# Optimization experiments

Measured on AMD Instinct MI355X. Metric: run time of the kernel, lower is better.

## Reference

```python
import jax, jax.numpy as jnp
import numpy as np

HID = 2048; NH = 16; NKV = 2; HD = 128; G = NH // NKV
SEC = (16, 24, 24)  # sums to 64 = HD/2
EPS = 1e-6
B, S = 2, 1024


def _reorder(table):
    # table: [3, B, S, HD]; interleave sections picking axis i%3 per chunk
    chunks = []
    idx = 0
    for _ in range(2):
        for sec in SEC:
            chunks.append(table[..., idx:idx + sec])
            idx += sec
    return jnp.concatenate([c[i % len(SEC)] for i, c in enumerate(chunks)], axis=-1)  # [B,S,HD]


def rotate_half(x):
    x1, x2 = jnp.split(x, 2, axis=-1)
    return jnp.concatenate((-x2, x1), axis=-1)


def rms_norm(x, gamma):
    var = jnp.mean(jnp.square(x), axis=-1, keepdims=True)
    return gamma * (x * jax.lax.rsqrt(var + EPS))


def setup_inputs() -> dict:
    key = jax.random.key(0)
    ks = jax.random.split(key, 12)
    x = jax.random.normal(ks[0], (B, S, HID), dtype=jnp.float32)
    ang = jax.random.uniform(ks[1], (3, B, S, HD), dtype=jnp.float32) * 6.28318
    cos = jnp.cos(ang)
    sin = jnp.sin(ang)
    mask = jnp.ones((B, S), dtype=jnp.float32)
    sc = 0.02
    q_w = jax.random.normal(ks[2], (HID, NH * HD), dtype=jnp.float32) * sc
    q_b = jnp.zeros((NH * HD,), dtype=jnp.float32)
    k_w = jax.random.normal(ks[3], (HID, NKV * HD), dtype=jnp.float32) * sc
    k_b = jnp.zeros((NKV * HD,), dtype=jnp.float32)
    v_w = jax.random.normal(ks[4], (HID, NKV * HD), dtype=jnp.float32) * sc
    v_b = jnp.zeros((NKV * HD,), dtype=jnp.float32)
    q_gamma = jnp.ones((HD,), dtype=jnp.float32)
    k_gamma = jnp.ones((HD,), dtype=jnp.float32)
    o_w = jax.random.normal(ks[5], (NH * HD, HID), dtype=jnp.float32) * sc
    return {"x": x, "cos": cos, "sin": sin, "mask": mask,
            "q_w": q_w, "q_b": q_b, "k_w": k_w, "k_b": k_b,
            "v_w": v_w, "v_b": v_b, "q_gamma": q_gamma, "k_gamma": k_gamma,
            "o_w": o_w}


def reference(x, cos, sin, mask, q_w, q_b, k_w, k_b, v_w, v_b, q_gamma, k_gamma, o_w):
    b, s, _ = x.shape
    # QKV projections
    q = (x @ q_w + q_b).reshape(b, s, NH, HD)
    k = (x @ k_w + k_b).reshape(b, s, NKV, HD)
    v = (x @ v_w + v_b).reshape(b, s, NKV, HD)
    # per-head RMSNorm on q, k
    q = rms_norm(q, q_gamma)
    k = rms_norm(k, k_gamma)
    q = jnp.transpose(q, (0, 2, 1, 3))  # [B,NH,S,HD]
    k = jnp.transpose(k, (0, 2, 1, 3))  # [B,NKV,S,HD]
    v = jnp.transpose(v, (0, 2, 1, 3))
    # multimodal RoPE
    cos_f = _reorder(cos)[:, None, :, :]  # [B,1,S,HD]
    sin_f = _reorder(sin)[:, None, :, :]
    q = q * cos_f + rotate_half(q) * sin_f
    k = k * cos_f + rotate_half(k) * sin_f
    # key-mask zeroing and effective lengths
    eff = mask.sum(axis=-1).astype(jnp.int32)  # [B]
    bm = mask[:, None, :, None]
    k = k * bm
    v = v * bm
    hist = (jnp.arange(s)[None, :] < eff[:, None]).astype(jnp.float32)  # [B,S]
    # GQA attention scores in fp32
    qg = q.reshape(b, NKV, G, s, HD)
    scores = jnp.einsum('bngqd,bnkd->bngqk', qg, k,
                        precision=jax.lax.Precision.HIGHEST) * (HD ** -0.5)
    scores = scores.reshape(b, NH, s, s)
    scores = scores + (1.0 - hist)[:, None, None, :] * -1e9
    causal = jnp.tril(jnp.ones((s, s), dtype=jnp.float32))
    scores = scores + (1.0 - causal)[None, None, :, :] * -1e9
    aw = jax.nn.softmax(scores, axis=-1)
    # weighted values
    out = jnp.einsum('bngqk,bnkd->bngqd', aw.reshape(b, NKV, G, s, s), v,
                     precision=jax.lax.Precision.HIGHEST)
    out = out.reshape(b, NH, s, HD)
    out = jnp.transpose(out, (0, 2, 1, 3)).reshape(b, s, NH * HD)
    return out @ o_w
```

## Files before the change

### kernel.cpp

```cpp
#include <hip/hip_runtime.h>

typedef __attribute__((ext_vector_type(8))) short bf16x8;
typedef __attribute__((ext_vector_type(4))) float f32x4;

#define MFMA16(a, b, c) __builtin_amdgcn_mfma_f32_16x16x32_bf16(a, b, c, 0, 0, 0)

__device__ inline short f2bf(float f) {
  union { float f; unsigned u; } v;
  v.f = f;
  unsigned r = v.u + 0x7FFF + ((v.u >> 16) & 1);
  return (short)(r >> 16);
}
__device__ inline float bf2f(short s) {
  union { unsigned u; float f; } v;
  v.u = ((unsigned)(unsigned short)s) << 16;
  return v.f;
}
#define GLD_LDS16(g, l)                                                        \
  __builtin_amdgcn_global_load_lds(                                            \
      (const __attribute__((address_space(1))) unsigned int*)(g),              \
      (__attribute__((address_space(3))) unsigned int*)(l), 16, 0, 0)

__device__ __forceinline__ void raw_barrier() {
  __asm__ volatile("" ::: "memory");
  __builtin_amdgcn_s_barrier();
  __asm__ volatile("" ::: "memory");
}

__global__ __launch_bounds__(256) void prep_kernel(
    const float* __restrict__ x, const float* __restrict__ q_w,
    const float* __restrict__ k_w, const float* __restrict__ v_w,
    const float* __restrict__ o_w, short* __restrict__ xb,
    short* __restrict__ wqkv_t, short* __restrict__ wo_t) {
  __shared__ float t[64][65];
  int bid = blockIdx.x;
  if (bid < 4096) {
    int i = (bid * 256 + threadIdx.x) * 4;
    float4 f = *(const float4*)&x[i];
    short4 o;
    o.x = f2bf(f.x); o.y = f2bf(f.y); o.z = f2bf(f.z); o.w = f2bf(f.w);
    *(short4*)&xb[i] = o;
    return;
  }
  bid -= 4096;
  const float* src;
  short* dst;
  int C, bx, by;
  if (bid < 1024) {
    src = q_w; dst = wqkv_t; C = 2048;
    bx = (bid & 31) * 64; by = (bid >> 5) * 64;
  } else if (bid < 1152) {
    bid -= 1024;
    src = k_w; dst = wqkv_t + (size_t)2048 * 2048; C = 256;
    bx = (bid & 3) * 64; by = (bid >> 2) * 64;
  } else if (bid < 1280) {
    bid -= 1152;
    src = v_w; dst = wqkv_t + (size_t)2304 * 2048; C = 256;
    bx = (bid & 3) * 64; by = (bid >> 2) * 64;
  } else {
    bid -= 1280;
    src = o_w; dst = wo_t; C = 2048;
    bx = (bid & 31) * 64; by = (bid >> 5) * 64;
  }
  const int R = 2048;
  const int tx = threadIdx.x & 15;
  const int ty = threadIdx.x >> 4;
#pragma unroll
  for (int i = 0; i < 4; i++) {
    int row = ty + i * 16;
    float4 f = *(const float4*)&src[(size_t)(by + row) * C + bx + tx * 4];
    t[row][tx * 4 + 0] = f.x;
    t[row][tx * 4 + 1] = f.y;
    t[row][tx * 4 + 2] = f.z;
    t[row][tx * 4 + 3] = f.w;
  }
  __syncthreads();
#pragma unroll
  for (int i = 0; i < 4; i++) {
    int c = ty + i * 16;
    short4 o;
    o.x = f2bf(t[tx * 4 + 0][c]);
    o.y = f2bf(t[tx * 4 + 1][c]);
    o.z = f2bf(t[tx * 4 + 2][c]);
    o.w = f2bf(t[tx * 4 + 3][c]);
    *(short4*)&dst[(size_t)(bx + c) * R + by + tx * 4] = o;
  }
}

__global__ __launch_bounds__(256) void gemm_db_kernel(const short* __restrict__ A,
                                                      const short* __restrict__ B,
                                                      float* __restrict__ C, int N,
                                                      int gx, int gy) {
  __shared__ __align__(16) short As[4][64 * 32];
  __shared__ __align__(16) short Bs[4][128 * 32];
  const int bid = blockIdx.x;
  const int xcd = bid & 7, idx = bid >> 3;
  const int colsPerX = gx >> 1, rowsPerX = gy >> 2;
  const int xt = (xcd & 1) * colsPerX + idx % colsPerX;
  const int yt = (xcd >> 1) * rowsPerX + idx / colsPerX;
  const int tid = threadIdx.x;
  const int lane = tid & 63, wave = tid >> 6;
  const int quad = lane >> 4, l16 = lane & 15;
  const int m0 = yt * 64, n0 = xt * 128;
  const int wm = (wave >> 1) * 32, wn = (wave & 1) * 64;
  const int r0 = tid >> 2, c0 = (tid & 3) * 8;
  const int ca = c0 ^ ((r0 & 3) << 3);
  const size_t arow = (size_t)(m0 + r0) * 2048;
  const size_t brow0 = (size_t)(n0 + r0) * 2048, brow1 = (size_t)(n0 + r0 + 64) * 2048;
  f32x4 acc[2][4];
#pragma unroll
  for (int mi = 0; mi < 2; mi++)
#pragma unroll
    for (int ni = 0; ni < 4; ni++) acc[mi][ni] = (f32x4){0.f, 0.f, 0.f, 0.f};

#pragma unroll
  for (int st = 0; st < 4; st++) {
    const int kk = st * 32 + ca;
    GLD_LDS16(&A[arow + kk], &As[st][r0 * 32 + c0]);
    GLD_LDS16(&B[brow0 + kk], &Bs[st][r0 * 32 + c0]);
    GLD_LDS16(&B[brow1 + kk], &Bs[st][(r0 + 64) * 32 + c0]);
  }

  const int sx = (l16 & 3) << 3;
  for (int p = 0; p < 32; p++) {
    if (p < 31) {
      __asm__ volatile("s_waitcnt vmcnt(6)" ::: "memory");
    } else {
      __asm__ volatile("s_waitcnt vmcnt(0)" ::: "memory");
    }
    raw_barrier();
#pragma unroll
    for (int j = 0; j < 2; j++) {
      const int cur = (2 * p + j) & 3;
      bf16x8 af[2], bfr[4];
#pragma unroll
      for (int mi = 0; mi < 2; mi++)
        af[mi] = *(const bf16x8*)&As[cur][(wm + mi * 16 + l16) * 32 + ((quad * 8) ^ sx)];
#pragma unroll
      for (int ni = 0; ni < 4; ni++)
        bfr[ni] = *(const bf16x8*)&Bs[cur][(wn + ni * 16 + l16) * 32 + ((quad * 8) ^ sx)];
#pragma unroll
      for (int mi = 0; mi < 2; mi++)
#pragma unroll
        for (int ni = 0; ni < 4; ni++)
          acc[mi][ni] = MFMA16(af[mi], bfr[ni], acc[mi][ni]);
    }
    __asm__ volatile("s_waitcnt lgkmcnt(0)" ::: "memory");
    raw_barrier();
    if (p < 30) {
#pragma unroll
      for (int j = 0; j < 2; j++) {
        const int st = 2 * p + 4 + j;
        const int slot = st & 3;
        const int kk = st * 32 + ca;
        GLD_LDS16(&A[arow + kk], &As[slot][r0 * 32 + c0]);
        GLD_LDS16(&B[brow0 + kk], &Bs[slot][r0 * 32 + c0]);
        GLD_LDS16(&B[brow1 + kk], &Bs[slot][(r0 + 64) * 32 + c0]);
      }
    }
  }
#pragma unroll
  for (int mi = 0; mi < 2; mi++)
#pragma unroll
    for (int ni = 0; ni < 4; ni++)
#pragma unroll
      for (int r = 0; r < 4; r++)
        C[(size_t)(m0 + wm + mi * 16 + quad * 4 + r) * N + n0 + wn + ni * 16 + l16] =
            acc[mi][ni][r];
}

__global__ __launch_bounds__(256) void postv_kernel(
    const float* __restrict__ qkv, const float* __restrict__ qbias,
    const float* __restrict__ kbias, const float* __restrict__ vbias,
    const float* __restrict__ qg, const float* __restrict__ kg,
    const float* __restrict__ cosb, const float* __restrict__ sinb,
    const float* __restrict__ maskp, short* __restrict__ qo, short* __restrict__ ko,
    short* __restrict__ vtb) {
  __shared__ short t[32][33];
  const int bid = blockIdx.x;
  if (bid < 9216) {
    const int rid = bid * 4 + (threadIdx.x >> 6);
    const int lane = threadIdx.x & 63;
    const int slot = rid >> 11;
    const int bs = rid & 2047;
    const int b = bs >> 10, s = bs & 1023;
    const float* row = qkv + (size_t)bs * 2560;
    int off;
    const float* bias;
    const float* gamma;
    if (slot < 16) { off = slot * 128; bias = qbias + slot * 128; gamma = qg; }
    else { off = 2048 + (slot - 16) * 128; bias = kbias + (slot - 16) * 128; gamma = kg; }
    float v0 = row[off + lane] + bias[lane];
    float v1 = row[off + 64 + lane] + bias[64 + lane];
    float ss = v0 * v0 + v1 * v1;
#pragma unroll
    for (int o = 1; o < 64; o <<= 1) ss += __shfl_xor(ss, o);
    float r = rsqrtf(ss * (1.0f / 128.0f) + 1e-6f);
    v0 = gamma[lane] * v0 * r;
    v1 = gamma[64 + lane] * v1 * r;
    int sel = (lane < 16) ? 0 : (lane < 40) ? 1 : 2;
    size_t ci = ((size_t)(sel * 2 + b) * 1024 + s) * 128 + lane;
    float c0 = cosb[ci], s0 = sinb[ci], c1 = cosb[ci + 64], s1 = sinb[ci + 64];
    float o0 = v0 * c0 - v1 * s0;
    float o1 = v1 * c1 + v0 * s1;
    if (slot >= 16) { float mk = maskp[bs]; o0 *= mk; o1 *= mk; }
    size_t oidx;
    short* optr;
    if (slot < 16) { oidx = (((size_t)(b * 16 + slot) * 1024) + s) * 128; optr = qo; }
    else { oidx = (((size_t)(b * 2 + (slot - 16)) * 1024) + s) * 128; optr = ko; }
    optr[oidx + lane] = f2bf(o0);
    optr[oidx + 64 + lane] = f2bf(o1);
    return;
  }
  const int b2 = bid - 9216;
  const int d0 = (b2 & 3) * 32;
  const int s0 = ((b2 >> 2) & 31) * 32;
  const int bz = b2 >> 7;
  const int bq = bz >> 1, kv = bz & 1;
  const int tx = threadIdx.x & 31;
  const int ty = threadIdx.x >> 5;
#pragma unroll
  for (int i = 0; i < 4; i++) {
    int s = s0 + ty + i * 8;
    float val = qkv[((size_t)(bq * 1024 + s)) * 2560 + 2304 + kv * 128 + d0 + tx] +
                vbias[kv * 128 + d0 + tx];
    t[ty + i * 8][tx] = f2bf(val * maskp[bq * 1024 + s]);
  }
  __syncthreads();
#pragma unroll
  for (int i = 0; i < 4; i++)
    vtb[((size_t)bz * 128 + d0 + ty + i * 8) * 1024 + s0 + tx] = t[tx][ty + i * 8];
}

__global__ __launch_bounds__(256) void attn_kernel(const short* __restrict__ Q,
                                                   const short* __restrict__ K,
                                                   const short* __restrict__ Vt_g,
                                                   short* __restrict__ po,
                                                   float* __restrict__ pml) {
  int x = blockIdx.x;
  const int h = blockIdx.y;
  const int b = blockIdx.z;
  int g = 0, base = 0;
  while (x >= base + 4 * (g + 1)) { base += 4 * (g + 1); g++; }
  const int r0 = x - base;
  const int qt = 4 * g + r0 / (g + 1);
  const int kc = r0 % (g + 1);
  int nsteps = qt - 4 * kc + 1;
  if (nsteps > 4) nsteps = 4;

  const int kv = h >> 3;
  const int tid = threadIdx.x;
  const int wave = tid >> 6, lane = tid & 63;
  const int quad = lane >> 4, l16 = lane & 15;
  __shared__ __align__(16) short Ks[2][64 * 128];
  __shared__ __align__(16) short Vs[2][128 * 64];
  __shared__ __align__(16) short Ps[4][16 * 72];

  const size_t qoff = (((size_t)(b * 16 + h) * 1024) + qt * 64 + wave * 16 + l16) * 128;
  bf16x8 aq[4];
#pragma unroll
  for (int kk = 0; kk < 4; kk++) aq[kk] = *(const bf16x8*)&Q[qoff + kk * 32 + quad * 8];

  f32x4 o[8];
#pragma unroll
  for (int i = 0; i < 8; i++) o[i] = (f32x4){0.f, 0.f, 0.f, 0.f};
  float l[4] = {0.f, 0.f, 0.f, 0.f};
  const int qrow0 = qt * 64 + wave * 16 + quad * 4;
  const size_t koff = ((size_t)(b * 2 + kv) * 1024) * 128;
  const size_t voff = koff;
  const float scale = 0.08838834764831845f;

#define STAGE_KV(bf, ks0)                                                          \
  {                                                                                \
    _Pragma("unroll") for (int it = 0; it < 4; it++) {                             \
      const int c = it * 256 + tid;                                                \
      const int row = c >> 4, sl = c & 15;                                         \
      GLD_LDS16(&K[koff + (size_t)((ks0) + row) * 128 + ((sl ^ (row & 7)) * 8)],   \
                &Ks[bf][c * 8]);                                                   \
      const int d = c >> 3, sv = c & 7;                                            \
      GLD_LDS16(&Vt_g[voff + (size_t)d * 1024 + (ks0) + ((sv ^ (d & 7)) * 8)],     \
                &Vs[bf][c * 8]);                                                   \
    }                                                                              \
  }

  STAGE_KV(0, kc * 256);

  for (int st = 0; st < nsteps; st++) {
    __asm__ volatile("s_waitcnt vmcnt(0)" ::: "memory");
    raw_barrier();
    if (st + 1 < nsteps) { STAGE_KV((st + 1) & 1, kc * 256 + (st + 1) * 64); }
    const int cb = st & 1;
    const int ks0 = kc * 256 + st * 64;
    f32x4 sc[4];
#pragma unroll
    for (int nt = 0; nt < 4; nt++) sc[nt] = (f32x4){0.f, 0.f, 0.f, 0.f};
#pragma unroll
    for (int nt = 0; nt < 4; nt++) {
      const int rr = nt * 16 + l16;
#pragma unroll
      for (int kk = 0; kk < 4; kk++) {
        bf16x8 bk = *(const bf16x8*)&Ks[cb][rr * 128 + (((kk * 4 + quad) ^ (rr & 7)) * 8)];
        sc[nt] = MFMA16(aq[kk], bk, sc[nt]);
      }
    }
    short* P = &Ps[wave][0];
#pragma unroll
    for (int nt = 0; nt < 4; nt++) {
      const int kcol = ks0 + nt * 16 + l16;
#pragma unroll
      for (int r = 0; r < 4; r++) {
        float p = (kcol > qrow0 + r) ? 0.f : __expf(fmaf(sc[nt][r], scale, -12.0f));
        l[r] += p;
        P[(quad * 4 + r) * 72 + nt * 16 + l16] = f2bf(p);
      }
    }
    __asm__ volatile("s_waitcnt lgkmcnt(0)" ::: "memory");
    bf16x8 pa0 = *(const bf16x8*)&P[l16 * 72 + quad * 8];
    bf16x8 pa1 = *(const bf16x8*)&P[l16 * 72 + 32 + quad * 8];
#pragma unroll
    for (int nt = 0; nt < 8; nt++) {
      const int rr = nt * 16 + l16;
      bf16x8 bv0 = *(const bf16x8*)&Vs[cb][rr * 64 + ((quad ^ (rr & 7)) * 8)];
      bf16x8 bv1 = *(const bf16x8*)&Vs[cb][rr * 64 + (((4 + quad) ^ (rr & 7)) * 8)];
      o[nt] = MFMA16(pa0, bv0, o[nt]);
      o[nt] = MFMA16(pa1, bv1, o[nt]);
    }
  }
#undef STAGE_KV
#pragma unroll
  for (int off = 1; off < 16; off <<= 1)
#pragma unroll
    for (int r = 0; r < 4; r++) l[r] += __shfl_xor(l[r], off);
  const int p = (b * 16 + h) * 40 + blockIdx.x;
  const int lrow = wave * 16 + quad * 4;
#pragma unroll
  for (int nt = 0; nt < 8; nt++)
#pragma unroll
    for (int r = 0; r < 4; r++)
      po[(size_t)p * 8192 + (size_t)(lrow + r) * 128 + nt * 16 + l16] = f2bf(o[nt][r]);
  if (l16 == 0) {
#pragma unroll
    for (int r = 0; r < 4; r++) pml[(size_t)p * 64 + lrow + r] = l[r];
  }
}

__global__ __launch_bounds__(256) void attn_combine_kernel(const short* __restrict__ po,
                                                           const float* __restrict__ pml,
                                                           short* __restrict__ attn) {
  const int qt = blockIdx.x, h = blockIdx.y, b = blockIdx.z;
  const int g = qt >> 2, nc = g + 1;
  const int x0 = 2 * g * (g + 1) + (qt & 3) * nc;
  const int row = threadIdx.x >> 2;
  const int d0 = (threadIdx.x & 3) * 32;
  const int pbase = (b * 16 + h) * 40 + x0;
  float denom = 0.f;
#pragma unroll
  for (int kc = 0; kc < 4; kc++)
    if (kc < nc) denom += pml[(size_t)(pbase + kc) * 64 + row];
  float inv = 1.f / denom;
  float acc[32];
#pragma unroll
  for (int j = 0; j < 32; j++) acc[j] = 0.f;
#pragma unroll
  for (int kc = 0; kc < 4; kc++)
    if (kc < nc) {
      const short* src = po + (size_t)(pbase + kc) * 8192 + (size_t)row * 128 + d0;
#pragma unroll
      for (int j = 0; j < 4; j++) {
        int4 v = *(const int4*)&src[j * 8];
        const short* vs = (const short*)&v;
#pragma unroll
        for (int e = 0; e < 8; e++) acc[j * 8 + e] += bf2f(vs[e]);
      }
    }
  short ob[32];
#pragma unroll
  for (int j = 0; j < 32; j++) ob[j] = f2bf(acc[j] * inv);
  short* dst = attn + ((size_t)(b * 1024 + qt * 64 + row)) * 2048 + h * 128 + d0;
#pragma unroll
  for (int j = 0; j < 4; j++) *(int4*)&dst[j * 8] = *(const int4*)&ob[j * 8];
}

extern "C" void kernel_launch(void* const* d_in, const int* in_sizes, int n_in,
                              void* d_out, int out_size, void* d_ws, size_t ws_size,
                              hipStream_t stream) {
  const float* x = (const float*)d_in[0];
  const float* cosb = (const float*)d_in[1];
  const float* sinb = (const float*)d_in[2];
  const float* mask = (const float*)d_in[3];
  const float* q_w = (const float*)d_in[4];
  const float* q_b = (const float*)d_in[5];
  const float* k_w = (const float*)d_in[6];
  const float* k_b = (const float*)d_in[7];
  const float* v_w = (const float*)d_in[8];
  const float* v_b = (const float*)d_in[9];
  const float* qg = (const float*)d_in[10];
  const float* kg = (const float*)d_in[11];
  const float* o_w = (const float*)d_in[12];
  float* out = (float*)d_out;

  char* ws = (char*)d_ws;
  short* wo_t = (short*)(ws);
  short* wqkv_t = (short*)(ws + ((size_t)8 << 20));
  float* pml = (float*)(ws + ((size_t)8 << 20));
  short* attn = (short*)(ws + ((size_t)9 << 20));
  short* xb = (short*)(ws + ((size_t)18 << 20));
  short* qb = xb;
  float* qkv_raw = (float*)(ws + ((size_t)26 << 20));
  short* po = (short*)(ws + ((size_t)26 << 20));
  short* kb = (short*)(ws + ((size_t)46 << 20));
  short* vtb = (short*)(ws + ((size_t)47 << 20));

  prep_kernel<<<6400, 256, 0, stream>>>(x, q_w, k_w, v_w, o_w, xb, wqkv_t, wo_t);
  gemm_db_kernel<<<640, 256, 0, stream>>>(xb, wqkv_t, qkv_raw, 2560, 20, 32);
  postv_kernel<<<9728, 256, 0, stream>>>(qkv_raw, q_b, k_b, v_b, qg, kg, cosb, sinb, mask,
                                         qb, kb, vtb);
  attn_kernel<<<dim3(40, 16, 2), 256, 0, stream>>>(qb, kb, vtb, po, pml);
  attn_combine_kernel<<<dim3(16, 16, 2), 256, 0, stream>>>(po, pml, attn);
  gemm_db_kernel<<<512, 256, 0, stream>>>(attn, wo_t, out, 2048, 16, 32);
}
```

Before: 223.9 us.

## Split-K the QKV GEMM into two halves and change LDS swizzle pattern

```diff
diff --git a/kernel.cpp b/kernel.cpp
--- a/kernel.cpp
+++ b/kernel.cpp
@@ -89,11 +89,18 @@
 
 __global__ __launch_bounds__(256) void gemm_db_kernel(const short* __restrict__ A,
                                                       const short* __restrict__ B,
-                                                      float* __restrict__ C, int N,
-                                                      int gx, int gy) {
+                                                      float* __restrict__ C,
+                                                      float* __restrict__ C2, int N,
+                                                      int gx, int gy, int P) {
   __shared__ __align__(16) short As[4][64 * 32];
   __shared__ __align__(16) short Bs[4][128 * 32];
-  const int bid = blockIdx.x;
+  int bid = blockIdx.x;
+  const int gxy = gx * gy;
+  int half = 0;
+  if (bid >= gxy) { half = 1; bid -= gxy; }
+  float* __restrict__ Cw = half ? C2 : C;
+  const short* __restrict__ Ab = A + half * (P * 64);
+  const short* __restrict__ Bb = B + half * (P * 64);
   const int xcd = bid & 7, idx = bid >> 3;
   const int colsPerX = gx >> 1, rowsPerX = gy >> 2;
   const int xt = (xcd & 1) * colsPerX + idx % colsPerX;
@@ -104,7 +111,7 @@
   const int m0 = yt * 64, n0 = xt * 128;
   const int wm = (wave >> 1) * 32, wn = (wave & 1) * 64;
   const int r0 = tid >> 2, c0 = (tid & 3) * 8;
-  const int ca = c0 ^ ((r0 & 3) << 3);
+  const int ca = ((tid & 3) ^ ((r0 >> 1) & 3)) * 8;
   const size_t arow = (size_t)(m0 + r0) * 2048;
   const size_t brow0 = (size_t)(n0 + r0) * 2048, brow1 = (size_t)(n0 + r0 + 64) * 2048;
   f32x4 acc[2][4];
@@ -116,14 +123,14 @@
 #pragma unroll
   for (int st = 0; st < 4; st++) {
     const int kk = st * 32 + ca;
-    GLD_LDS16(&A[arow + kk], &As[st][r0 * 32 + c0]);
-    GLD_LDS16(&B[brow0 + kk], &Bs[st][r0 * 32 + c0]);
-    GLD_LDS16(&B[brow1 + kk], &Bs[st][(r0 + 64) * 32 + c0]);
-  }
-
-  const int sx = (l16 & 3) << 3;
-  for (int p = 0; p < 32; p++) {
-    if (p < 31) {
+    GLD_LDS16(&Ab[arow + kk], &As[st][r0 * 32 + c0]);
+    GLD_LDS16(&Bb[brow0 + kk], &Bs[st][r0 * 32 + c0]);
+    GLD_LDS16(&Bb[brow1 + kk], &Bs[st][(r0 + 64) * 32 + c0]);
+  }
+
+  const int sx = (l16 >> 1) & 3;
+  for (int p = 0; p < P; p++) {
+    if (p < P - 1) {
       __asm__ volatile("s_waitcnt vmcnt(6)" ::: "memory");
     } else {
       __asm__ volatile("s_waitcnt vmcnt(0)" ::: "memory");
@@ -135,10 +142,10 @@
       bf16x8 af[2], bfr[4];
 #pragma unroll
       for (int mi = 0; mi < 2; mi++)
-        af[mi] = *(const bf16x8*)&As[cur][(wm + mi * 16 + l16) * 32 + ((quad * 8) ^ sx)];
+        af[mi] = *(const bf16x8*)&As[cur][(wm + mi * 16 + l16) * 32 + ((quad ^ sx) * 8)];
 #pragma unroll
       for (int ni = 0; ni < 4; ni++)
-        bfr[ni] = *(const bf16x8*)&Bs[cur][(wn + ni * 16 + l16) * 32 + ((quad * 8) ^ sx)];
+        bfr[ni] = *(const bf16x8*)&Bs[cur][(wn + ni * 16 + l16) * 32 + ((quad ^ sx) * 8)];
 #pragma unroll
       for (int mi = 0; mi < 2; mi++)
 #pragma unroll
@@ -147,15 +154,15 @@
     }
     __asm__ volatile("s_waitcnt lgkmcnt(0)" ::: "memory");
     raw_barrier();
-    if (p < 30) {
+    if (p < P - 2) {
 #pragma unroll
       for (int j = 0; j < 2; j++) {
         const int st = 2 * p + 4 + j;
         const int slot = st & 3;
         const int kk = st * 32 + ca;
-        GLD_LDS16(&A[arow + kk], &As[slot][r0 * 32 + c0]);
-        GLD_LDS16(&B[brow0 + kk], &Bs[slot][r0 * 32 + c0]);
-        GLD_LDS16(&B[brow1 + kk], &Bs[slot][(r0 + 64) * 32 + c0]);
+        GLD_LDS16(&Ab[arow + kk], &As[slot][r0 * 32 + c0]);
+        GLD_LDS16(&Bb[brow0 + kk], &Bs[slot][r0 * 32 + c0]);
+        GLD_LDS16(&Bb[brow1 + kk], &Bs[slot][(r0 + 64) * 32 + c0]);
       }
     }
   }
@@ -165,17 +172,17 @@
     for (int ni = 0; ni < 4; ni++)
 #pragma unroll
       for (int r = 0; r < 4; r++)
-        C[(size_t)(m0 + wm + mi * 16 + quad * 4 + r) * N + n0 + wn + ni * 16 + l16] =
+        Cw[(size_t)(m0 + wm + mi * 16 + quad * 4 + r) * N + n0 + wn + ni * 16 + l16] =
             acc[mi][ni][r];
 }
 
 __global__ __launch_bounds__(256) void postv_kernel(
-    const float* __restrict__ qkv, const float* __restrict__ qbias,
-    const float* __restrict__ kbias, const float* __restrict__ vbias,
-    const float* __restrict__ qg, const float* __restrict__ kg,
-    const float* __restrict__ cosb, const float* __restrict__ sinb,
-    const float* __restrict__ maskp, short* __restrict__ qo, short* __restrict__ ko,
-    short* __restrict__ vtb) {
+    const float* __restrict__ qkv, const float* __restrict__ qkv2,
+    const float* __restrict__ qbias, const float* __restrict__ kbias,
+    const float* __restrict__ vbias, const float* __restrict__ qg,
+    const float* __restrict__ kg, const float* __restrict__ cosb,
+    const float* __restrict__ sinb, const float* __restrict__ maskp,
+    short* __restrict__ qo, short* __restrict__ ko, short* __restrict__ vtb) {
   __shared__ short t[32][33];
   const int bid = blockIdx.x;
   if (bid < 9216) {
@@ -185,13 +192,14 @@
     const int bs = rid & 2047;
     const int b = bs >> 10, s = bs & 1023;
     const float* row = qkv + (size_t)bs * 2560;
+    const float* row2 = qkv2 + (size_t)bs * 2560;
     int off;
     const float* bias;
     const float* gamma;
     if (slot < 16) { off = slot * 128; bias = qbias + slot * 128; gamma = qg; }
     else { off = 2048 + (slot - 16) * 128; bias = kbias + (slot - 16) * 128; gamma = kg; }
-    float v0 = row[off + lane] + bias[lane];
-    float v1 = row[off + 64 + lane] + bias[64 + lane];
+    float v0 = row[off + lane] + row2[off + lane] + bias[lane];
+    float v1 = row[off + 64 + lane] + row2[off + 64 + lane] + bias[64 + lane];
     float ss = v0 * v0 + v1 * v1;
 #pragma unroll
     for (int o = 1; o < 64; o <<= 1) ss += __shfl_xor(ss, o);
@@ -222,8 +230,8 @@
 #pragma unroll
   for (int i = 0; i < 4; i++) {
     int s = s0 + ty + i * 8;
-    float val = qkv[((size_t)(bq * 1024 + s)) * 2560 + 2304 + kv * 128 + d0 + tx] +
-                vbias[kv * 128 + d0 + tx];
+    size_t qi = ((size_t)(bq * 1024 + s)) * 2560 + 2304 + kv * 128 + d0 + tx;
+    float val = qkv[qi] + qkv2[qi] + vbias[kv * 128 + d0 + tx];
     t[ty + i * 8][tx] = f2bf(val * maskp[bq * 1024 + s]);
   }
   __syncthreads();
@@ -410,12 +418,13 @@
   short* po = (short*)(ws + ((size_t)26 << 20));
   short* kb = (short*)(ws + ((size_t)46 << 20));
   short* vtb = (short*)(ws + ((size_t)47 << 20));
+  float* qkv_raw2 = (float*)(ws + ((size_t)48 << 20));
 
   prep_kernel<<<6400, 256, 0, stream>>>(x, q_w, k_w, v_w, o_w, xb, wqkv_t, wo_t);
-  gemm_db_kernel<<<640, 256, 0, stream>>>(xb, wqkv_t, qkv_raw, 2560, 20, 32);
-  postv_kernel<<<9728, 256, 0, stream>>>(qkv_raw, q_b, k_b, v_b, qg, kg, cosb, sinb, mask,
-                                         qb, kb, vtb);
+  gemm_db_kernel<<<1280, 256, 0, stream>>>(xb, wqkv_t, qkv_raw, qkv_raw2, 2560, 20, 32, 16);
+  postv_kernel<<<9728, 256, 0, stream>>>(qkv_raw, qkv_raw2, q_b, k_b, v_b, qg, kg, cosb,
+                                         sinb, mask, qb, kb, vtb);
   attn_kernel<<<dim3(40, 16, 2), 256, 0, stream>>>(qb, kb, vtb, po, pml);
   attn_combine_kernel<<<dim3(16, 16, 2), 256, 0, stream>>>(po, pml, attn);
-  gemm_db_kernel<<<512, 256, 0, stream>>>(attn, wo_t, out, 2048, 16, 32);
-}
+  gemm_db_kernel<<<512, 256, 0, stream>>>(attn, wo_t, out, out, 2048, 16, 32, 32);
+}
```

Measured after the change: 227.6 us. Within noise of the previous version (+1.7%).
